# Kernel optimization log

Measured on AMD Instinct MI355X. Metric: run time of the kernel, lower is better.

The kernel has to match this reference:

```python
import jax, jax.numpy as jnp
import numpy as np
import math

N_HEAD = 16
HEAD_DIM = 64
N_EMBD = N_HEAD * HEAD_DIM  # 1024


def _alibi_slopes(n_heads):
    def pow2(n):
        start = 2.0 ** (-2.0 ** (-(math.log2(n) - 3)))
        return [start * (start ** i) for i in range(n)]
    if n_heads & (n_heads - 1) == 0:
        s = pow2(n_heads)
    else:
        cp2 = 2 ** math.floor(math.log2(n_heads))
        s = pow2(cp2)
        extra_base = 2.0 ** (-2.0 ** (-(math.log2(2 * cp2) - 3)))
        s += [extra_base * (extra_base ** i) for i in range(n_heads - cp2)]
        s = s[:n_heads]
    return jnp.asarray(np.array(s, dtype=np.float32))


def setup_inputs() -> dict:
    key = jax.random.key(0)
    k1, k2, k3, k4 = jax.random.split(key, 4)
    B, T = 2, 2048
    x = jax.random.normal(k1, (B, T, N_EMBD), dtype=jnp.float32)
    # c_attn weight for q,k (use_v=True -> 2*n_embd outputs), no bias
    W_attn = jax.random.normal(k2, (N_EMBD, 2 * N_EMBD), dtype=jnp.float32) * 0.02
    v_tmp = jax.random.normal(k3, (N_HEAD, N_HEAD), dtype=jnp.float32) * 0.02
    proj_tmp = jax.random.normal(k4, (N_HEAD, N_HEAD), dtype=jnp.float32) * 0.02
    return {"x": x, "W_attn": W_attn, "v_tmp": v_tmp, "proj_tmp": proj_tmp}


def reference(x, W_attn, v_tmp, proj_tmp):
    B, T, C = x.shape
    H, D = N_HEAD, HEAD_DIM
    scale = 1.0 / math.sqrt(D)

    qk = x @ W_attn  # (B,T,2C)
    q, k = qk[..., :C], qk[..., C:]
    q = q.reshape(B, T, H, D).transpose(0, 2, 1, 3)  # (B,H,T,D)
    k = k.reshape(B, T, H, D).transpose(0, 2, 1, 3)

    # V via Kronecker-lifted matrix: x @ kron(v_tmp, I_D)
    # block structure => mix head channels: out[...,j,d] = sum_i x[...,i,d]*v_tmp[i,j]
    xh = x.reshape(B, T, H, D)
    v = jnp.einsum('btid,ij->btjd', xh, v_tmp)  # (B,T,H,D)

    scores = jnp.einsum('bhqd,bhkd->bhqk', q, k) * scale  # (B,H,T,T)

    # ALiBi bias + causal mask
    pos = jnp.arange(T, dtype=jnp.float32)
    rel = pos[None, :] - pos[:, None]  # (T,T), mem - ctx
    slopes = _alibi_slopes(H)
    bias = slopes[:, None, None] * rel[None, :, :]
    causal = pos[None, :] <= pos[:, None]
    bias = jnp.where(causal[None, :, :], bias, -jnp.inf)
    scores = scores + bias[None]

    att = jax.nn.softmax(scores, axis=-1)
    y = jnp.einsum('bhqk,bkhd->bqhd', att, v)  # (B,T,H,D)

    # output proj via kron(proj_tmp, I_D).T: out[...,i,d] = sum_j y[...,j,d]*proj_tmp[i,j]
    y = jnp.einsum('btjd,ij->btid', y, proj_tmp)
    return y.reshape(B, T, C)
```

## Files before the change

kernel.cpp:

```cpp
#include <hip/hip_runtime.h>

typedef __attribute__((ext_vector_type(8))) __bf16 bf16x8;
typedef __attribute__((ext_vector_type(8))) unsigned short u16x8;
typedef __attribute__((ext_vector_type(4))) float f32x4;

#define LOG2E 1.4426950408889634f

#define GLDS16(gp, lp)                                                \
  __builtin_amdgcn_global_load_lds(                                   \
      (const __attribute__((address_space(1))) void*)(gp),            \
      (__attribute__((address_space(3))) void*)(lp), 16, 0, 0)

__device__ __forceinline__ unsigned short f2b(float f) {
  return __builtin_bit_cast(unsigned short, (__bf16)f);
}
__device__ __forceinline__ float b2f(unsigned short h) {
  return __uint_as_float(((unsigned)h) << 16);
}

__global__ __launch_bounds__(256) void k_xv(const float* __restrict__ x,
                                            const float* __restrict__ vt,
                                            unsigned short* __restrict__ xb,
                                            unsigned short* __restrict__ vb) {
  __shared__ float s_vt[256];
  s_vt[threadIdx.x] = vt[threadIdx.x];
  __syncthreads();
  int g = blockIdx.x * 256 + threadIdx.x;
  int bt = g >> 6, d = g & 63;
  const float* xp = x + (size_t)bt * 1024 + d;
  float xi[16];
#pragma unroll
  for (int i = 0; i < 16; ++i) xi[i] = xp[i * 64];
#pragma unroll
  for (int i = 0; i < 16; ++i) xb[(size_t)bt * 1024 + i * 64 + d] = f2b(xi[i]);
#pragma unroll
  for (int j = 0; j < 16; ++j) {
    float s = 0.f;
#pragma unroll
    for (int i = 0; i < 16; ++i) s += xi[i] * s_vt[i * 16 + j];
    vb[(size_t)bt * 1024 + j * 64 + d] = f2b(s);
  }
}

__global__ __launch_bounds__(256) void k_trans_w(const float* __restrict__ W,
                                                 unsigned short* __restrict__ Wt) {
  __shared__ unsigned short tile[64][65];
  int n0 = blockIdx.x * 64;
  int k0 = blockIdx.y * 64;
  int tx = threadIdx.x & 63, ty = threadIdx.x >> 6;
#pragma unroll
  for (int r = 0; r < 16; ++r) {
    int kk = ty * 16 + r;
    tile[kk][tx] = f2b(W[(size_t)(k0 + kk) * 2048 + n0 + tx]);
  }
  __syncthreads();
#pragma unroll
  for (int r = 0; r < 16; ++r) {
    int nn = ty * 16 + r;
    Wt[(size_t)(n0 + nn) * 1024 + k0 + tx] = tile[tx][nn];
  }
}

__global__ __launch_bounds__(256) void k_gemm_qk(const unsigned short* __restrict__ A,
                                                 const unsigned short* __restrict__ Bt,
                                                 unsigned short* __restrict__ C) {
  __shared__ unsigned short As[128 * 32];
  __shared__ unsigned short Bs[128 * 32];
  const int K = 1024;
  int m0 = blockIdx.x * 128;
  int n0 = blockIdx.y * 128;
  int tid = threadIdx.x;
  int w = tid >> 6, lane = tid & 63;
  int lq = lane & 15, lk8 = (lane >> 4) * 8;
  int wr = (w >> 1) * 64, wc = (w & 1) * 64;
  f32x4 acc[4][4];
#pragma unroll
  for (int i = 0; i < 4; ++i)
#pragma unroll
    for (int j = 0; j < 4; ++j)
#pragma unroll
      for (int r = 0; r < 4; ++r) acc[i][j][r] = 0.f;

  for (int kk = 0; kk < K; kk += 32) {
    __syncthreads();
#pragma unroll
    for (int i = 0; i < 2; ++i) {
      int c = tid + 256 * i;
      int row = c >> 2, col = (c & 3) * 8;
      GLDS16(A + (size_t)(m0 + row) * K + kk + col, As + c * 8);
      GLDS16(Bt + (size_t)(n0 + row) * K + kk + col, Bs + c * 8);
    }
    __syncthreads();
    bf16x8 af[4], bf[4];
#pragma unroll
    for (int i = 0; i < 4; ++i) af[i] = *(const bf16x8*)(As + (wr + i * 16 + lq) * 32 + lk8);
#pragma unroll
    for (int j = 0; j < 4; ++j) bf[j] = *(const bf16x8*)(Bs + (wc + j * 16 + lq) * 32 + lk8);
#pragma unroll
    for (int i = 0; i < 4; ++i)
#pragma unroll
      for (int j = 0; j < 4; ++j)
        acc[i][j] = __builtin_amdgcn_mfma_f32_16x16x32_bf16(af[i], bf[j], acc[i][j], 0, 0, 0);
  }
#pragma unroll
  for (int i = 0; i < 4; ++i)
#pragma unroll
    for (int j = 0; j < 4; ++j)
#pragma unroll
      for (int r = 0; r < 4; ++r) {
        int m = m0 + wr + i * 16 + (lane >> 4) * 4 + r;
        int n = n0 + wc + j * 16 + lq;
        C[(size_t)m * 2048 + n] = f2b(acc[i][j][r]);
      }
}

__global__ __launch_bounds__(256) void k_vtrans(const unsigned short* __restrict__ vb,
                                                unsigned short* __restrict__ Vt) {
  __shared__ unsigned short tile[64][65];
  int t0 = blockIdx.x * 64;
  int c0 = blockIdx.y * 64;
  int b = blockIdx.z;
  int tx = threadIdx.x & 63, ty = threadIdx.x >> 6;
#pragma unroll
  for (int r = 0; r < 16; ++r) {
    int tt = ty * 16 + r;
    tile[tt][tx] = vb[((size_t)b * 2048 + t0 + tt) * 1024 + c0 + tx];
  }
  __syncthreads();
#pragma unroll
  for (int r = 0; r < 16; ++r) {
    int cc = ty * 16 + r;
    Vt[((size_t)b * 1024 + c0 + cc) * 2048 + t0 + tx] = tile[tx][cc];
  }
}

__global__ __launch_bounds__(256) void k_flash(const unsigned short* __restrict__ qkb,
                                               const unsigned short* __restrict__ Vt,
                                               unsigned short* __restrict__ y) {
  __shared__ unsigned short Ks[2][2][64 * 32];
  __shared__ unsigned short Vs[2][2][64 * 32];
  __shared__ unsigned short Pbuf[4][16 * 64];
  int id = blockIdx.x;
  int xcd = id & 7, s = id >> 3;
  int g = xcd + 8 * (s >> 4);
  int j = s & 15;
  int hd = g & 15, b = g >> 4;
  int tid = threadIdx.x;
  int w = tid >> 6, lane = tid & 63;
  int quad = lane >> 4, lq = lane & 15, lk8 = quad * 8;
  int rs = tid >> 2, cs = (tid & 3) * 8;
  const size_t rowb = (size_t)b * 2048;
  const size_t vrow = ((size_t)b * 1024 + hd * 64 + rs) * 2048 + cs;
  const size_t krow = ((rowb + rs) << 11) + 1024 + hd * 64 + cs;

  float slope = exp2f(-0.5f * (float)(hd + 1));
  const float c1 = 0.125f * LOG2E;
  const float c2 = slope * LOG2E;
  const float SHIFT = 16.0f;

  bf16x8 ones;
#pragma unroll
  for (int i = 0; i < 8; ++i) ones[i] = (__bf16)1.0f;

#pragma unroll 1
  for (int pass = 0; pass < 2; ++pass) {
    int qt = pass ? (31 - j) : j;
    int q0 = qt * 64;
    int qg = q0 + w * 16 + lq;

    bf16x8 qf0 = *(const bf16x8*)(qkb + ((rowb + qg) << 11) + hd * 64 + lk8);
    bf16x8 qf1 = *(const bf16x8*)(qkb + ((rowb + qg) << 11) + hd * 64 + 32 + lk8);

    int qrow_base = q0 + w * 16 + quad * 4;

    float base_b[4][4];
#pragma unroll
    for (int s4 = 0; s4 < 4; ++s4)
#pragma unroll
      for (int r = 0; r < 4; ++r)
        base_b[s4][r] = c2 * (float)(s4 * 16 + lq - qrow_base - r) - SHIFT;

    f32x4 o[4], o4;
#pragma unroll
    for (int r = 0; r < 4; ++r) o4[r] = 0.f;
#pragma unroll
    for (int jj = 0; jj < 4; ++jj)
#pragma unroll
      for (int r = 0; r < 4; ++r) o[jj][r] = 0.f;

    __syncthreads();
    GLDS16(qkb + krow,      &Ks[0][0][rs * 32 + cs]);
    GLDS16(qkb + krow + 32, &Ks[0][1][rs * 32 + cs]);
    GLDS16(Vt + vrow,       &Vs[0][0][rs * 32 + cs]);
    GLDS16(Vt + vrow + 32,  &Vs[0][1][rs * 32 + cs]);
    __syncthreads();
    int cur = 0;

#pragma unroll 1
    for (int kt = 0; kt <= qt; ++kt) {
      int k0 = kt * 64;
      if (kt < qt) {
        size_t koff = (size_t)(k0 + 64);
        int nxt = cur ^ 1;
        GLDS16(qkb + krow + (koff << 11),      &Ks[nxt][0][rs * 32 + cs]);
        GLDS16(qkb + krow + (koff << 11) + 32, &Ks[nxt][1][rs * 32 + cs]);
        GLDS16(Vt + vrow + koff,               &Vs[nxt][0][rs * 32 + cs]);
        GLDS16(Vt + vrow + koff + 32,          &Vs[nxt][1][rs * 32 + cs]);
      }
      bf16x8 kc[4][2];
#pragma unroll
      for (int s4 = 0; s4 < 4; ++s4) {
        u16x8 t0 = *(const u16x8*)(&Ks[cur][0][(s4 * 16 + lq) * 32 + lk8]);
        u16x8 t1 = *(const u16x8*)(&Ks[cur][1][(s4 * 16 + lq) * 32 + lk8]);
        kc[s4][0] = __builtin_bit_cast(bf16x8, t0);
        kc[s4][1] = __builtin_bit_cast(bf16x8, t1);
      }
      f32x4 S[4];
#pragma unroll
      for (int s4 = 0; s4 < 4; ++s4) {
        f32x4 a;
#pragma unroll
        for (int r = 0; r < 4; ++r) a[r] = 0.f;
        a = __builtin_amdgcn_mfma_f32_16x16x32_bf16(qf0, kc[s4][0], a, 0, 0, 0);
        a = __builtin_amdgcn_mfma_f32_16x16x32_bf16(qf1, kc[s4][1], a, 0, 0, 0);
        S[s4] = a;
      }
      float bk = c2 * (float)k0;
      float p[4][4];
      if (kt == qt) {
#pragma unroll
        for (int s4 = 0; s4 < 4; ++s4) {
          int kg = k0 + s4 * 16 + lq;
#pragma unroll
          for (int r = 0; r < 4; ++r) {
            int qr = qrow_base + r;
            float v = S[s4][r] * c1 + (base_b[s4][r] + bk);
            v = (kg <= qr) ? v : -1e30f;
            p[s4][r] = exp2f(v);
          }
        }
      } else {
#pragma unroll
        for (int s4 = 0; s4 < 4; ++s4) {
#pragma unroll
          for (int r = 0; r < 4; ++r) {
            float v = S[s4][r] * c1 + (base_b[s4][r] + bk);
            p[s4][r] = exp2f(v);
          }
        }
      }
#pragma unroll
      for (int s4 = 0; s4 < 4; ++s4) {
        int cg = (s4 ^ quad) << 4;
#pragma unroll
        for (int r = 0; r < 4; ++r)
          Pbuf[w][(quad * 4 + r) * 64 + cg + lq] = f2b(p[s4][r]);
      }
      int g0 = ((quad >> 1) ^ (lq >> 2)) << 4;
      int g1 = ((2 | (quad >> 1)) ^ (lq >> 2)) << 4;
      int sub = (quad & 1) * 8;
      u16x8 t0 = *(const u16x8*)(&Pbuf[w][lq * 64 + g0 + sub]);
      u16x8 t1 = *(const u16x8*)(&Pbuf[w][lq * 64 + g1 + sub]);
      bf16x8 pf0 = __builtin_bit_cast(bf16x8, t0);
      bf16x8 pf1 = __builtin_bit_cast(bf16x8, t1);
#pragma unroll
      for (int jj = 0; jj < 4; ++jj) {
        u16x8 v0 = *(const u16x8*)(&Vs[cur][0][(jj * 16 + lq) * 32 + lk8]);
        u16x8 v1 = *(const u16x8*)(&Vs[cur][1][(jj * 16 + lq) * 32 + lk8]);
        bf16x8 vf0 = __builtin_bit_cast(bf16x8, v0);
        bf16x8 vf1 = __builtin_bit_cast(bf16x8, v1);
        o[jj] = __builtin_amdgcn_mfma_f32_16x16x32_bf16(pf0, vf0, o[jj], 0, 0, 0);
        o[jj] = __builtin_amdgcn_mfma_f32_16x16x32_bf16(pf1, vf1, o[jj], 0, 0, 0);
        if (jj == 0) {
          o4 = __builtin_amdgcn_mfma_f32_16x16x32_bf16(pf0, ones, o4, 0, 0, 0);
          o4 = __builtin_amdgcn_mfma_f32_16x16x32_bf16(pf1, ones, o4, 0, 0, 0);
        }
      }
      if (kt < qt) {
        __syncthreads();
        cur ^= 1;
      }
    }
#pragma unroll
    for (int r = 0; r < 4; ++r) {
      float inv = 1.0f / o4[r];
      int qr = qrow_base + r;
#pragma unroll
      for (int jj = 0; jj < 4; ++jj)
        y[((rowb + qr) << 10) + hd * 64 + jj * 16 + lq] = f2b(o[jj][r] * inv);
    }
  }
}

__global__ __launch_bounds__(256) void k_proj(const unsigned short* __restrict__ yb,
                                              const float* __restrict__ pt,
                                              float* __restrict__ out) {
  __shared__ float s_pt[256];
  s_pt[threadIdx.x] = pt[threadIdx.x];
  __syncthreads();
  int g = blockIdx.x * 256 + threadIdx.x;
  int bt = g >> 6, d = g & 63;
  float yj[16];
#pragma unroll
  for (int j = 0; j < 16; ++j) yj[j] = b2f(yb[(size_t)bt * 1024 + j * 64 + d]);
#pragma unroll
  for (int i = 0; i < 16; ++i) {
    float s = 0.f;
#pragma unroll
    for (int j = 0; j < 16; ++j) s += yj[j] * s_pt[i * 16 + j];
    out[(size_t)bt * 1024 + i * 64 + d] = s;
  }
}

extern "C" void kernel_launch(void* const* d_in, const int* in_sizes, int n_in,
                              void* d_out, int out_size, void* d_ws, size_t ws_size,
                              hipStream_t stream) {
  const float* x  = (const float*)d_in[0];
  const float* W  = (const float*)d_in[1];
  const float* vt = (const float*)d_in[2];
  const float* pt = (const float*)d_in[3];
  float* out = (float*)d_out;

  char* ws = (char*)d_ws;
  unsigned short* xb  = (unsigned short*)(ws);
  unsigned short* Wt  = (unsigned short*)(ws + (8u  << 20));
  unsigned short* qkb = (unsigned short*)(ws + (12u << 20));
  unsigned short* vb  = (unsigned short*)(ws + (28u << 20));
  unsigned short* Vtr = (unsigned short*)(ws + (36u << 20));
  unsigned short* yb  = xb;

  k_xv     <<<1024, 256, 0, stream>>>(x, vt, xb, vb);
  k_trans_w<<<dim3(32, 16), 256, 0, stream>>>(W, Wt);
  k_gemm_qk<<<dim3(32, 16), 256, 0, stream>>>(xb, Wt, qkb);
  k_vtrans <<<dim3(32, 16, 2), 256, 0, stream>>>(vb, Vtr);
  k_flash  <<<512, 256, 0, stream>>>(qkb, Vtr, yb);
  k_proj   <<<1024, 256, 0, stream>>>(yb, pt, out);
}
```

Measured before the change: 164.9 us.

## Fuse paired causal query tiles into one KV sweep sharing K/V loads

The flash kernel used to process its two query tiles (j and 31-j) in two separate passes, each streaming K/V from the start. They are now handled together: for key tiles up to qtA, each loaded K/V tile feeds both query tiles, and the sweep then continues for tile B alone. This cuts K/V global loads and barriers by roughly a third and interleaves two independent MFMA/softmax chains. The cost is more registers (two accumulator sets), a doubled P buffer in shared memory, and possibly lower occupancy.

```diff
diff --git a/kernel.cpp b/kernel.cpp
--- a/kernel.cpp
+++ b/kernel.cpp
@@ -139,12 +139,12 @@
                                                unsigned short* __restrict__ y) {
   __shared__ unsigned short Ks[2][2][64 * 32];
   __shared__ unsigned short Vs[2][2][64 * 32];
-  __shared__ unsigned short Pbuf[4][16 * 64];
+  __shared__ unsigned short Pbuf[8][16 * 64];
   int id = blockIdx.x;
   int xcd = id & 7, s = id >> 3;
-  int g = xcd + 8 * (s >> 4);
+  int grp = xcd + 8 * (s >> 4);
   int j = s & 15;
-  int hd = g & 15, b = g >> 4;
+  int hd = grp & 15, b = grp >> 4;
   int tid = threadIdx.x;
   int w = tid >> 6, lane = tid & 63;
   int quad = lane >> 4, lq = lane & 15, lk8 = quad * 8;
@@ -162,132 +162,185 @@
 #pragma unroll
   for (int i = 0; i < 8; ++i) ones[i] = (__bf16)1.0f;
 
+  const int qtA = j, qtB = 31 - j;
+  int qgA = qtA * 64 + w * 16 + lq;
+  int qgB = qtB * 64 + w * 16 + lq;
+  bf16x8 qfA0 = *(const bf16x8*)(qkb + ((rowb + qgA) << 11) + hd * 64 + lk8);
+  bf16x8 qfA1 = *(const bf16x8*)(qkb + ((rowb + qgA) << 11) + hd * 64 + 32 + lk8);
+  bf16x8 qfB0 = *(const bf16x8*)(qkb + ((rowb + qgB) << 11) + hd * 64 + lk8);
+  bf16x8 qfB1 = *(const bf16x8*)(qkb + ((rowb + qgB) << 11) + hd * 64 + 32 + lk8);
+  const int qbaseA = qtA * 64 + w * 16 + quad * 4;
+  const int qbaseB = qtB * 64 + w * 16 + quad * 4;
+
+  float rowA_[4], rowB_[4];
+#pragma unroll
+  for (int r = 0; r < 4; ++r) {
+    rowA_[r] = -c2 * (float)(qbaseA + r) - SHIFT;
+    rowB_[r] = -c2 * (float)(qbaseB + r) - SHIFT;
+  }
+
+  int g0 = ((quad >> 1) ^ (lq >> 2)) << 4;
+  int g1 = ((2 | (quad >> 1)) ^ (lq >> 2)) << 4;
+  int sub = (quad & 1) * 8;
+
+  f32x4 oA[4], oB[4], o4A, o4B;
+#pragma unroll
+  for (int r = 0; r < 4; ++r) { o4A[r] = 0.f; o4B[r] = 0.f; }
+#pragma unroll
+  for (int jj = 0; jj < 4; ++jj)
+#pragma unroll
+    for (int r = 0; r < 4; ++r) { oA[jj][r] = 0.f; oB[jj][r] = 0.f; }
+
+  auto qk2 = [&](bf16x8 q0v, bf16x8 q1v, bf16x8 (*kc)[2], f32x4* S) {
+#pragma unroll
+    for (int s4 = 0; s4 < 4; ++s4) {
+      f32x4 a;
+#pragma unroll
+      for (int r = 0; r < 4; ++r) a[r] = 0.f;
+      a = __builtin_amdgcn_mfma_f32_16x16x32_bf16(q0v, kc[s4][0], a, 0, 0, 0);
+      a = __builtin_amdgcn_mfma_f32_16x16x32_bf16(q1v, kc[s4][1], a, 0, 0, 0);
+      S[s4] = a;
+    }
+  };
+  auto chain = [&](const f32x4* S, const float* rw, const float* colv, bool diag,
+                   int qb, int k0, int pslot, bf16x8& pf0, bf16x8& pf1) {
+    float p[4][4];
+#pragma unroll
+    for (int s4 = 0; s4 < 4; ++s4)
+#pragma unroll
+      for (int r = 0; r < 4; ++r) {
+        float v = S[s4][r] * c1 + (colv[s4] + rw[r]);
+        if (diag) {
+          int kg = k0 + s4 * 16 + lq;
+          v = (kg <= qb + r) ? v : -1e30f;
+        }
+        p[s4][r] = exp2f(v);
+      }
+#pragma unroll
+    for (int s4 = 0; s4 < 4; ++s4) {
+      int cg = (s4 ^ quad) << 4;
+#pragma unroll
+      for (int r = 0; r < 4; ++r)
+        Pbuf[pslot][(quad * 4 + r) * 64 + cg + lq] = f2b(p[s4][r]);
+    }
+    u16x8 t0 = *(const u16x8*)(&Pbuf[pslot][lq * 64 + g0 + sub]);
+    u16x8 t1 = *(const u16x8*)(&Pbuf[pslot][lq * 64 + g1 + sub]);
+    pf0 = __builtin_bit_cast(bf16x8, t0);
+    pf1 = __builtin_bit_cast(bf16x8, t1);
+  };
+
+  GLDS16(qkb + krow,      &Ks[0][0][rs * 32 + cs]);
+  GLDS16(qkb + krow + 32, &Ks[0][1][rs * 32 + cs]);
+  GLDS16(Vt + vrow,       &Vs[0][0][rs * 32 + cs]);
+  GLDS16(Vt + vrow + 32,  &Vs[0][1][rs * 32 + cs]);
+  __syncthreads();
+  int cur = 0;
+
 #pragma unroll 1
-  for (int pass = 0; pass < 2; ++pass) {
-    int qt = pass ? (31 - j) : j;
-    int q0 = qt * 64;
-    int qg = q0 + w * 16 + lq;
-
-    bf16x8 qf0 = *(const bf16x8*)(qkb + ((rowb + qg) << 11) + hd * 64 + lk8);
-    bf16x8 qf1 = *(const bf16x8*)(qkb + ((rowb + qg) << 11) + hd * 64 + 32 + lk8);
-
-    int qrow_base = q0 + w * 16 + quad * 4;
-
-    float base_b[4][4];
-#pragma unroll
-    for (int s4 = 0; s4 < 4; ++s4)
-#pragma unroll
-      for (int r = 0; r < 4; ++r)
-        base_b[s4][r] = c2 * (float)(s4 * 16 + lq - qrow_base - r) - SHIFT;
-
-    f32x4 o[4], o4;
-#pragma unroll
-    for (int r = 0; r < 4; ++r) o4[r] = 0.f;
-#pragma unroll
-    for (int jj = 0; jj < 4; ++jj)
-#pragma unroll
-      for (int r = 0; r < 4; ++r) o[jj][r] = 0.f;
-
+  for (int kt = 0; kt <= qtA; ++kt) {
+    int k0 = kt * 64;
+    {
+      size_t koff = (size_t)(k0 + 64);
+      int nxt = cur ^ 1;
+      GLDS16(qkb + krow + (koff << 11),      &Ks[nxt][0][rs * 32 + cs]);
+      GLDS16(qkb + krow + (koff << 11) + 32, &Ks[nxt][1][rs * 32 + cs]);
+      GLDS16(Vt + vrow + koff,               &Vs[nxt][0][rs * 32 + cs]);
+      GLDS16(Vt + vrow + koff + 32,          &Vs[nxt][1][rs * 32 + cs]);
+    }
+    bf16x8 kc[4][2];
+#pragma unroll
+    for (int s4 = 0; s4 < 4; ++s4) {
+      u16x8 t0 = *(const u16x8*)(&Ks[cur][0][(s4 * 16 + lq) * 32 + lk8]);
+      u16x8 t1 = *(const u16x8*)(&Ks[cur][1][(s4 * 16 + lq) * 32 + lk8]);
+      kc[s4][0] = __builtin_bit_cast(bf16x8, t0);
+      kc[s4][1] = __builtin_bit_cast(bf16x8, t1);
+    }
+    f32x4 SA[4], SB[4];
+    qk2(qfA0, qfA1, kc, SA);
+    qk2(qfB0, qfB1, kc, SB);
+    float colv[4];
+#pragma unroll
+    for (int s4 = 0; s4 < 4; ++s4) colv[s4] = c2 * (float)(k0 + s4 * 16 + lq);
+    bf16x8 pfA0, pfA1, pfB0, pfB1;
+    if (kt == qtA) chain(SA, rowA_, colv, true,  qbaseA, k0, w,     pfA0, pfA1);
+    else           chain(SA, rowA_, colv, false, qbaseA, k0, w,     pfA0, pfA1);
+    chain(SB, rowB_, colv, false, qbaseB, k0, 4 + w, pfB0, pfB1);
+#pragma unroll
+    for (int jj = 0; jj < 4; ++jj) {
+      u16x8 v0 = *(const u16x8*)(&Vs[cur][0][(jj * 16 + lq) * 32 + lk8]);
+      u16x8 v1 = *(const u16x8*)(&Vs[cur][1][(jj * 16 + lq) * 32 + lk8]);
+      bf16x8 vf0 = __builtin_bit_cast(bf16x8, v0);
+      bf16x8 vf1 = __builtin_bit_cast(bf16x8, v1);
+      oA[jj] = __builtin_amdgcn_mfma_f32_16x16x32_bf16(pfA0, vf0, oA[jj], 0, 0, 0);
+      oA[jj] = __builtin_amdgcn_mfma_f32_16x16x32_bf16(pfA1, vf1, oA[jj], 0, 0, 0);
+      oB[jj] = __builtin_amdgcn_mfma_f32_16x16x32_bf16(pfB0, vf0, oB[jj], 0, 0, 0);
+      oB[jj] = __builtin_amdgcn_mfma_f32_16x16x32_bf16(pfB1, vf1, oB[jj], 0, 0, 0);
+      if (jj == 0) {
+        o4A = __builtin_amdgcn_mfma_f32_16x16x32_bf16(pfA0, ones, o4A, 0, 0, 0);
+        o4A = __builtin_amdgcn_mfma_f32_16x16x32_bf16(pfA1, ones, o4A, 0, 0, 0);
+        o4B = __builtin_amdgcn_mfma_f32_16x16x32_bf16(pfB0, ones, o4B, 0, 0, 0);
+        o4B = __builtin_amdgcn_mfma_f32_16x16x32_bf16(pfB1, ones, o4B, 0, 0, 0);
+      }
+    }
     __syncthreads();
-    GLDS16(qkb + krow,      &Ks[0][0][rs * 32 + cs]);
-    GLDS16(qkb + krow + 32, &Ks[0][1][rs * 32 + cs]);
-    GLDS16(Vt + vrow,       &Vs[0][0][rs * 32 + cs]);
-    GLDS16(Vt + vrow + 32,  &Vs[0][1][rs * 32 + cs]);
-    __syncthreads();
-    int cur = 0;
+    cur ^= 1;
+  }
 
 #pragma unroll 1
-    for (int kt = 0; kt <= qt; ++kt) {
-      int k0 = kt * 64;
-      if (kt < qt) {
-        size_t koff = (size_t)(k0 + 64);
-        int nxt = cur ^ 1;
-        GLDS16(qkb + krow + (koff << 11),      &Ks[nxt][0][rs * 32 + cs]);
-        GLDS16(qkb + krow + (koff << 11) + 32, &Ks[nxt][1][rs * 32 + cs]);
-        GLDS16(Vt + vrow + koff,               &Vs[nxt][0][rs * 32 + cs]);
-        GLDS16(Vt + vrow + koff + 32,          &Vs[nxt][1][rs * 32 + cs]);
+  for (int kt = qtA + 1; kt <= qtB; ++kt) {
+    int k0 = kt * 64;
+    if (kt < qtB) {
+      size_t koff = (size_t)(k0 + 64);
+      int nxt = cur ^ 1;
+      GLDS16(qkb + krow + (koff << 11),      &Ks[nxt][0][rs * 32 + cs]);
+      GLDS16(qkb + krow + (koff << 11) + 32, &Ks[nxt][1][rs * 32 + cs]);
+      GLDS16(Vt + vrow + koff,               &Vs[nxt][0][rs * 32 + cs]);
+      GLDS16(Vt + vrow + koff + 32,          &Vs[nxt][1][rs * 32 + cs]);
+    }
+    bf16x8 kc[4][2];
+#pragma unroll
+    for (int s4 = 0; s4 < 4; ++s4) {
+      u16x8 t0 = *(const u16x8*)(&Ks[cur][0][(s4 * 16 + lq) * 32 + lk8]);
+      u16x8 t1 = *(const u16x8*)(&Ks[cur][1][(s4 * 16 + lq) * 32 + lk8]);
+      kc[s4][0] = __builtin_bit_cast(bf16x8, t0);
+      kc[s4][1] = __builtin_bit_cast(bf16x8, t1);
+    }
+    f32x4 SB[4];
+    qk2(qfB0, qfB1, kc, SB);
+    float colv[4];
+#pragma unroll
+    for (int s4 = 0; s4 < 4; ++s4) colv[s4] = c2 * (float)(k0 + s4 * 16 + lq);
+    bf16x8 pfB0, pfB1;
+    if (kt == qtB) chain(SB, rowB_, colv, true,  qbaseB, k0, 4 + w, pfB0, pfB1);
+    else           chain(SB, rowB_, colv, false, qbaseB, k0, 4 + w, pfB0, pfB1);
+#pragma unroll
+    for (int jj = 0; jj < 4; ++jj) {
+      u16x8 v0 = *(const u16x8*)(&Vs[cur][0][(jj * 16 + lq) * 32 + lk8]);
+      u16x8 v1 = *(const u16x8*)(&Vs[cur][1][(jj * 16 + lq) * 32 + lk8]);
+      bf16x8 vf0 = __builtin_bit_cast(bf16x8, v0);
+      bf16x8 vf1 = __builtin_bit_cast(bf16x8, v1);
+      oB[jj] = __builtin_amdgcn_mfma_f32_16x16x32_bf16(pfB0, vf0, oB[jj], 0, 0, 0);
+      oB[jj] = __builtin_amdgcn_mfma_f32_16x16x32_bf16(pfB1, vf1, oB[jj], 0, 0, 0);
+      if (jj == 0) {
+        o4B = __builtin_amdgcn_mfma_f32_16x16x32_bf16(pfB0, ones, o4B, 0, 0, 0);
+        o4B = __builtin_amdgcn_mfma_f32_16x16x32_bf16(pfB1, ones, o4B, 0, 0, 0);
       }
-      bf16x8 kc[4][2];
-#pragma unroll
-      for (int s4 = 0; s4 < 4; ++s4) {
-        u16x8 t0 = *(const u16x8*)(&Ks[cur][0][(s4 * 16 + lq) * 32 + lk8]);
-        u16x8 t1 = *(const u16x8*)(&Ks[cur][1][(s4 * 16 + lq) * 32 + lk8]);
-        kc[s4][0] = __builtin_bit_cast(bf16x8, t0);
-        kc[s4][1] = __builtin_bit_cast(bf16x8, t1);
-      }
-      f32x4 S[4];
-#pragma unroll
-      for (int s4 = 0; s4 < 4; ++s4) {
-        f32x4 a;
-#pragma unroll
-        for (int r = 0; r < 4; ++r) a[r] = 0.f;
-        a = __builtin_amdgcn_mfma_f32_16x16x32_bf16(qf0, kc[s4][0], a, 0, 0, 0);
-        a = __builtin_amdgcn_mfma_f32_16x16x32_bf16(qf1, kc[s4][1], a, 0, 0, 0);
-        S[s4] = a;
-      }
-      float bk = c2 * (float)k0;
-      float p[4][4];
-      if (kt == qt) {
-#pragma unroll
-        for (int s4 = 0; s4 < 4; ++s4) {
-          int kg = k0 + s4 * 16 + lq;
-#pragma unroll
-          for (int r = 0; r < 4; ++r) {
-            int qr = qrow_base + r;
-            float v = S[s4][r] * c1 + (base_b[s4][r] + bk);
-            v = (kg <= qr) ? v : -1e30f;
-            p[s4][r] = exp2f(v);
-          }
-        }
-      } else {
-#pragma unroll
-        for (int s4 = 0; s4 < 4; ++s4) {
-#pragma unroll
-          for (int r = 0; r < 4; ++r) {
-            float v = S[s4][r] * c1 + (base_b[s4][r] + bk);
-            p[s4][r] = exp2f(v);
-          }
-        }
-      }
-#pragma unroll
-      for (int s4 = 0; s4 < 4; ++s4) {
-        int cg = (s4 ^ quad) << 4;
-#pragma unroll
-        for (int r = 0; r < 4; ++r)
-          Pbuf[w][(quad * 4 + r) * 64 + cg + lq] = f2b(p[s4][r]);
-      }
-      int g0 = ((quad >> 1) ^ (lq >> 2)) << 4;
-      int g1 = ((2 | (quad >> 1)) ^ (lq >> 2)) << 4;
-      int sub = (quad & 1) * 8;
-      u16x8 t0 = *(const u16x8*)(&Pbuf[w][lq * 64 + g0 + sub]);
-      u16x8 t1 = *(const u16x8*)(&Pbuf[w][lq * 64 + g1 + sub]);
-      bf16x8 pf0 = __builtin_bit_cast(bf16x8, t0);
-      bf16x8 pf1 = __builtin_bit_cast(bf16x8, t1);
-#pragma unroll
-      for (int jj = 0; jj < 4; ++jj) {
-        u16x8 v0 = *(const u16x8*)(&Vs[cur][0][(jj * 16 + lq) * 32 + lk8]);
-        u16x8 v1 = *(const u16x8*)(&Vs[cur][1][(jj * 16 + lq) * 32 + lk8]);
-        bf16x8 vf0 = __builtin_bit_cast(bf16x8, v0);
-        bf16x8 vf1 = __builtin_bit_cast(bf16x8, v1);
-        o[jj] = __builtin_amdgcn_mfma_f32_16x16x32_bf16(pf0, vf0, o[jj], 0, 0, 0);
-        o[jj] = __builtin_amdgcn_mfma_f32_16x16x32_bf16(pf1, vf1, o[jj], 0, 0, 0);
-        if (jj == 0) {
-          o4 = __builtin_amdgcn_mfma_f32_16x16x32_bf16(pf0, ones, o4, 0, 0, 0);
-          o4 = __builtin_amdgcn_mfma_f32_16x16x32_bf16(pf1, ones, o4, 0, 0, 0);
-        }
-      }
-      if (kt < qt) {
-        __syncthreads();
-        cur ^= 1;
-      }
-    }
-#pragma unroll
-    for (int r = 0; r < 4; ++r) {
-      float inv = 1.0f / o4[r];
-      int qr = qrow_base + r;
-#pragma unroll
-      for (int jj = 0; jj < 4; ++jj)
-        y[((rowb + qr) << 10) + hd * 64 + jj * 16 + lq] = f2b(o[jj][r] * inv);
+    }
+    if (kt < qtB) {
+      __syncthreads();
+      cur ^= 1;
+    }
+  }
+
+#pragma unroll
+  for (int r = 0; r < 4; ++r) {
+    float invA = 1.0f / o4A[r];
+    float invB = 1.0f / o4B[r];
+    int qrA = qbaseA + r, qrB = qbaseB + r;
+#pragma unroll
+    for (int jj = 0; jj < 4; ++jj) {
+      y[((rowb + qrA) << 10) + hd * 64 + jj * 16 + lq] = f2b(oA[jj][r] * invA);
+      y[((rowb + qrB) << 10) + hd * 64 + jj * 16 + lq] = f2b(oB[jj][r] * invB);
     }
   }
 }
```

Measured after the change: 171.0 us. 3.6% more time.
